# Performance work log

Hardware: AMD Instinct MI355X
Metric: run time of the kernel (lower is better)

## Reference

```python
import jax, jax.numpy as jnp
import numpy as np
from jax import lax

LATENT = 64
NUM_EMB = 512
BETA = 0.25
DN = ('NCHW', 'OIHW', 'NCHW')


def conv(x, w, b, stride, pad):
    y = lax.conv_general_dilated(x, w, (stride, stride), [(pad, pad), (pad, pad)],
                                 dimension_numbers=DN)
    return y + b[None, :, None, None]


def tconv(x, w, b, stride, pad, opad):
    # torch ConvTranspose2d(k=3, stride, padding=pad, output_padding=opad)
    # == dilated conv with lhs_dilation=stride, padding (k-1-pad, k-1-pad+opad),
    #    spatially-flipped kernel. w is stored OIHW (out, in, kh, kw).
    k = w.shape[2]
    lo, hi = k - 1 - pad, k - 1 - pad + opad
    y = lax.conv_general_dilated(x, w[:, :, ::-1, ::-1], (1, 1), [(lo, hi), (lo, hi)],
                                 lhs_dilation=(stride, stride), dimension_numbers=DN)
    return y + b[None, :, None, None]


def vector_quantize(z, codebook):
    # z: (B, D, H, W); codebook: (K, D)
    B, D, H, W = z.shape
    flat = z.transpose(0, 2, 3, 1).reshape(-1, D)  # (BHW, D)
    d = (jnp.sum(flat ** 2, axis=1, keepdims=True)
         + jnp.sum(codebook ** 2, axis=1)
         - 2.0 * flat @ codebook.T)  # (BHW, K)
    idx = jnp.argmin(d, axis=1)
    q = codebook[idx].reshape(B, H, W, D).transpose(0, 3, 1, 2)  # (B, D, H, W)
    commitment = jnp.mean((lax.stop_gradient(q) - z) ** 2)
    codebook_loss = jnp.mean((q - lax.stop_gradient(z)) ** 2)
    loss = BETA * commitment + codebook_loss
    q_ste = z + lax.stop_gradient(q - z)  # straight-through estimator
    return q_ste, loss


def setup_inputs() -> dict:
    key = jax.random.key(0)
    ks = jax.random.split(key, 16)
    f32 = jnp.float32
    inp = {
        'x': jax.random.uniform(ks[0], (1024, 1, 50, 50), dtype=f32),
        'enc_w1': jax.random.normal(ks[1], (32, 1, 3, 3), f32) * 0.1,
        'enc_b1': jnp.zeros((32,), f32),
        'enc_w2': jax.random.normal(ks[2], (64, 32, 3, 3), f32) * 0.05,
        'enc_b2': jnp.zeros((64,), f32),
        'enc_w3': jax.random.normal(ks[3], (LATENT, 64, 1, 1), f32) * 0.1,
        'enc_b3': jnp.zeros((LATENT,), f32),
        'codebook': jax.random.uniform(ks[4], (NUM_EMB, LATENT), dtype=f32),
        'dec_w1': jax.random.normal(ks[5], (64, LATENT, 3, 3), f32) * 0.05,
        'dec_b1': jnp.zeros((64,), f32),
        'dec_w2': jax.random.normal(ks[6], (32, 64, 3, 3), f32) * 0.05,
        'dec_b2': jnp.zeros((32,), f32),
        'dec_w3': jax.random.normal(ks[7], (1, 32, 3, 3), f32) * 0.05,
        'dec_b3': jnp.zeros((1,), f32),
    }
    return inp


def reference(x, enc_w1, enc_b1, enc_w2, enc_b2, enc_w3, enc_b3, codebook,
              dec_w1, dec_b1, dec_w2, dec_b2, dec_w3, dec_b3):
    # encoder: (B,1,50,50) -> (B,LATENT,13,13)
    h = jax.nn.relu(conv(x, enc_w1, enc_b1, 2, 1))
    h = jax.nn.relu(conv(h, enc_w2, enc_b2, 2, 1))
    z = conv(h, enc_w3, enc_b3, 1, 0)
    q, vq_loss = vector_quantize(z, codebook)
    # decoder: 13 -> 25 -> 50
    h = jax.nn.relu(tconv(q, dec_w1, dec_b1, 2, 1, 0))
    h = jax.nn.relu(tconv(h, dec_w2, dec_b2, 2, 1, 1))
    x_recon = jax.nn.sigmoid(conv(h, dec_w3, dec_b3, 1, 1))
    return x_recon, vq_loss
```

## Files before the change

### kernel.cpp

```cpp
#include <hip/hip_runtime.h>
#include <math.h>


typedef __attribute__((ext_vector_type(8))) short s8v;
typedef __attribute__((ext_vector_type(4))) float f4v;
typedef __attribute__((ext_vector_type(4))) int i4v;
typedef __attribute__((ext_vector_type(4))) short s4v;

__device__ inline unsigned short f2bf(float f) {
    unsigned u = __builtin_bit_cast(unsigned, f);
    return (unsigned short)((u + 0x7fffu + ((u >> 16) & 1u)) >> 16);
}
__device__ inline float bf2f(unsigned short h) {
    return __builtin_bit_cast(float, ((unsigned)h) << 16);
}

__global__ __launch_bounds__(256) void k_prep_all(
        const float* __restrict__ cb,  const float* __restrict__ ew2,
        const float* __restrict__ ew3, const float* __restrict__ dw1,
        const float* __restrict__ dw2,
        unsigned short* __restrict__ cbm, unsigned short* __restrict__ wB2n,
        unsigned short* __restrict__ wB1, unsigned short* __restrict__ wB2,
        unsigned short* __restrict__ wB3, float* __restrict__ cn,
        float* __restrict__ loss) {
    int i = blockIdx.x * 256 + threadIdx.x;
    if (i < 98304) {
        int j = i & 7, lane = (i >> 3) & 63;
        int kc = (i >> 9) % 6, nt = (i >> 9) / 6;
        int n = nt * 16 + (lane & 15);
        int k = kc * 32 + ((lane >> 4) << 3) + j;
        int seg = k >> 6, kk = k & 63;
        float c = cb[n * 64 + kk];
        unsigned short ch = f2bf(c);
        cbm[i] = (seg == 1) ? f2bf(c - bf2f(ch)) : ch;
    } else if (i < 153600) {
        int q = i - 98304;
        int j = q & 7, lane = (q >> 3) & 63;
        int kc = (q >> 9) % 27, nt = (q >> 9) / 27;
        int k = kc * 32 + ((lane >> 4) << 3) + j;
        int co = nt * 16 + (lane & 15);
        int part = (k < 288) ? 0 : (k < 576) ? 1 : 0;
        int kk = (k < 288) ? k : (k < 576) ? k - 288 : k - 576;
        int tap = kk >> 5, ci = kk & 31;
        float v = ew2[(co * 32 + ci) * 9 + tap];
        unsigned short hi = f2bf(v);
        wB2n[q] = part ? f2bf(v - bf2f(hi)) : hi;
    } else if (i < 219136) {
        int q = i - 153600;
        int j = q & 7, l = (q >> 3) & 63, kc = (q >> 9) & 7, nt = q >> 12;
        int n = nt * 16 + (l & 15), k = kc * 32 + (l >> 4) * 8 + j;
        int cls = n >> 6, co = n & 63, p = k >> 6, ci = k & 63;
        int jh = -1, jw = -1;
        if (cls == 0)      { if (p == 0) { jh = 1; jw = 1; } }
        else if (cls == 1) { if (p == 1) { jh = 1; jw = 0; } else if (p == 0) { jh = 1; jw = 2; } }
        else if (cls == 2) { if (p == 2) { jh = 0; jw = 1; } else if (p == 0) { jh = 2; jw = 1; } }
        else { if (p == 3) { jh = 0; jw = 0; } else if (p == 2) { jh = 0; jw = 2; }
               else if (p == 1) { jh = 2; jw = 0; } else { jh = 2; jw = 2; } }
        float v = (jh >= 0) ? dw1[((co * 64 + ci) * 3 + jh) * 3 + jw] : 0.f;
        wB1[q] = f2bf(v);
    } else if (i < 251904) {
        int q = i - 219136;
        int j = q & 7, l = (q >> 3) & 63, kc = (q >> 9) & 7, nt = q >> 12;
        int n = nt * 16 + (l & 15), k = kc * 32 + (l >> 4) * 8 + j;
        int cls = n >> 5, co = n & 31, p = k >> 6, ci = k & 63;
        int jh = -1, jw = -1;
        if (cls == 0)      { if (p == 0) { jh = 1; jw = 1; } }
        else if (cls == 1) { if (p == 1) { jh = 1; jw = 0; } else if (p == 0) { jh = 1; jw = 2; } }
        else if (cls == 2) { if (p == 2) { jh = 0; jw = 1; } else if (p == 0) { jh = 2; jw = 1; } }
        else { if (p == 3) { jh = 0; jw = 0; } else if (p == 2) { jh = 0; jw = 2; }
               else if (p == 1) { jh = 2; jw = 0; } else { jh = 2; jw = 2; } }
        float v = (jh >= 0) ? dw2[((co * 64 + ci) * 3 + jh) * 3 + jw] : 0.f;
        wB2[q] = f2bf(v);
    } else if (i < 264192) {
        int q = i - 251904;
        int j = q & 7, lane = (q >> 3) & 63;
        int kc = (q >> 9) % 6, nt = (q >> 9) / 6;
        int k = kc * 32 + ((lane >> 4) << 3) + j;
        int n = nt * 16 + (lane & 15);
        int part = (k < 64) ? 0 : (k < 128) ? 1 : 0;
        int kk = (k < 64) ? k : (k < 128) ? k - 64 : k - 128;
        float v = ew3[n * 64 + kk];
        unsigned short hi = f2bf(v);
        wB3[q] = part ? f2bf(v - bf2f(hi)) : hi;
    } else if (i < 264704) {
        int k = i - 264192;
        const float* r = cb + k * 64;
        float s = 0.f;
#pragma unroll
        for (int c = 0; c < 64; ++c) s += r[c] * r[c];
        cn[k] = s;
    } else if (i == 264704) {
        *loss = 0.f;
    }
}

__global__ __launch_bounds__(256) void k_conv1(const float* __restrict__ x,
                                               const float* __restrict__ w,
                                               const float* __restrict__ b,
                                               unsigned short* __restrict__ h1,
                                               int total) {
    __shared__ float4 wl4[72];
    float* wl = (float*)wl4;
    int tid = threadIdx.x;
    for (int t = tid; t < 288; t += 256) {
        int tap = t >> 5, co = t & 31;
        wl[t] = w[co * 9 + tap];
    }
    __syncthreads();
    int pix = blockIdx.x * 256 + tid;
    if (pix >= total) return;
    int n = pix / 625, p = pix % 625, oh = p / 25, ow = p % 25;
    const float* xp = x + (size_t)n * 2500;
    float4 a[8];
#pragma unroll
    for (int j = 0; j < 8; ++j) a[j] = ((const float4*)b)[j];
#pragma unroll
    for (int kh = 0; kh < 3; ++kh) {
        int ih = 2 * oh - 1 + kh;
        if ((unsigned)ih >= 50u) continue;
#pragma unroll
        for (int kw = 0; kw < 3; ++kw) {
            int iw = 2 * ow - 1 + kw;
            if ((unsigned)iw >= 50u) continue;
            float v = xp[ih * 50 + iw];
            int tap = kh * 3 + kw;
#pragma unroll
            for (int j = 0; j < 8; ++j) {
                float4 ww = wl4[tap * 8 + j];
                a[j].x += v * ww.x; a[j].y += v * ww.y;
                a[j].z += v * ww.z; a[j].w += v * ww.w;
            }
        }
    }
    unsigned short hi[32], lo[32];
#pragma unroll
    for (int j = 0; j < 8; ++j) {
        float vv[4] = {a[j].x, a[j].y, a[j].z, a[j].w};
#pragma unroll
        for (int e = 0; e < 4; ++e) {
            float v = fmaxf(vv[e], 0.f);
            unsigned short h = f2bf(v);
            hi[j * 4 + e] = h;
            lo[j * 4 + e] = f2bf(v - bf2f(h));
        }
    }
    i4v* op = (i4v*)(h1 + (size_t)pix * 64);
#pragma unroll
    for (int g = 0; g < 4; ++g) {
        i4v ph, pl;
#pragma unroll
        for (int e = 0; e < 4; ++e) {
            int b0 = g * 8 + e * 2;
            ph[e] = (int)((unsigned)hi[b0] | ((unsigned)hi[b0 + 1] << 16));
            pl[e] = (int)((unsigned)lo[b0] | ((unsigned)lo[b0 + 1] << 16));
        }
        op[g] = ph;
        op[4 + g] = pl;
    }
}

__global__ __launch_bounds__(256) void k_enc_m(const unsigned short* __restrict__ h1,
                                               const unsigned short* __restrict__ B2n,
                                               const unsigned short* __restrict__ B3,
                                               const float* __restrict__ b2,
                                               const float* __restrict__ b3,
                                               unsigned short* __restrict__ z, int npix) {
    __shared__ short a1[16 * 872];
    __shared__ short a2[16 * 200];
    __shared__ short czs[16 * 136];
    int tid = threadIdx.x, blk = blockIdx.x;
    {
        int m = tid >> 4, chunk = tid & 15;
        if (chunk < 9) {
            int pix = blk * 16 + m;
            i4v vh[4], vl[4];
#pragma unroll
            for (int g = 0; g < 4; ++g) {
                vh[g] = (i4v){0, 0, 0, 0};
                vl[g] = (i4v){0, 0, 0, 0};
            }
            if (pix < npix) {
                int n = pix / 169, p = pix % 169, oh = p / 13, ow = p % 13;
                int kh = chunk / 3, kw = chunk % 3;
                int ih = 2 * oh - 1 + kh, iw = 2 * ow - 1 + kw;
                if (((unsigned)ih < 25u) && ((unsigned)iw < 25u)) {
                    const i4v* ip = (const i4v*)(h1 + (((size_t)n * 25 + ih) * 25 + iw) * 64);
#pragma unroll
                    for (int g = 0; g < 4; ++g) { vh[g] = ip[g]; vl[g] = ip[4 + g]; }
                }
            }
            short* row = a1 + m * 872 + chunk * 32;
            i4v* d0 = (i4v*)row;
            i4v* d1 = (i4v*)(row + 288);
            i4v* d2 = (i4v*)(row + 576);
#pragma unroll
            for (int g = 0; g < 4; ++g) { d0[g] = vh[g]; d1[g] = vh[g]; d2[g] = vl[g]; }
        }
    }
    __syncthreads();
    int wave = tid >> 6, lane = tid & 63;
    int arow1 = (lane & 15) * 872 + (lane >> 4) * 8;
    f4v acc = (f4v){0.f, 0.f, 0.f, 0.f};
#pragma unroll
    for (int kc = 0; kc < 27; ++kc) {
        s8v a = *(const s8v*)(a1 + arow1 + kc * 32);
        s8v b = *(const s8v*)((const short*)B2n + ((size_t)((wave * 27 + kc) * 64 + lane)) * 8);
        acc = __builtin_amdgcn_mfma_f32_16x16x32_bf16(a, b, acc, 0, 0, 0);
    }
    {
        float bv = b2[wave * 16 + (lane & 15)];
        int n = wave * 16 + (lane & 15);
#pragma unroll
        for (int r = 0; r < 4; ++r) {
            int m = (lane >> 4) * 4 + r;
            float h = fmaxf(acc[r] + bv, 0.f);
            unsigned short hh = f2bf(h);
            unsigned short ll = f2bf(h - bf2f(hh));
            a2[m * 200 + n] = (short)hh;
            a2[m * 200 + 64 + n] = (short)hh;
            a2[m * 200 + 128 + n] = (short)ll;
        }
    }
    __syncthreads();
    int arow2 = (lane & 15) * 200 + (lane >> 4) * 8;
    f4v acc2 = (f4v){0.f, 0.f, 0.f, 0.f};
#pragma unroll
    for (int kc = 0; kc < 6; ++kc) {
        s8v a = *(const s8v*)(a2 + arow2 + kc * 32);
        s8v b = *(const s8v*)((const short*)B3 + ((size_t)((wave * 6 + kc) * 64 + lane)) * 8);
        acc2 = __builtin_amdgcn_mfma_f32_16x16x32_bf16(a, b, acc2, 0, 0, 0);
    }
    {
        float bv = b3[wave * 16 + (lane & 15)];
        int n = wave * 16 + (lane & 15);
#pragma unroll
        for (int r = 0; r < 4; ++r) {
            int m = (lane >> 4) * 4 + r;
            float v = acc2[r] + bv;
            unsigned short hh = f2bf(v);
            czs[m * 136 + n] = (short)hh;
            czs[m * 136 + 64 + n] = (short)f2bf(v - bf2f(hh));
        }
    }
    __syncthreads();
    {
        int m = tid >> 4, t = tid & 15;
        int pix = blk * 16 + m;
        if (pix < npix)
            *(i4v*)(z + (size_t)pix * 128 + t * 8) = *(i4v*)(czs + m * 136 + t * 8);
    }
}

__global__ __launch_bounds__(256, 2) void k_vq_m(const unsigned short* __restrict__ z,
                                                 const float* __restrict__ cb,
                                                 const unsigned short* __restrict__ cbm,
                                                 const float* __restrict__ cn,
                                                 unsigned short* __restrict__ q,
                                                 float* __restrict__ lpart, int npix) {
    __shared__ short a_lds[128 * 136];
    __shared__ int bkf[128];
    __shared__ float lred4[4];
    int tid = threadIdx.x, blk = blockIdx.x;
    {
        const i4v* src = (const i4v*)(z + (size_t)blk * 128 * 128);
#pragma unroll
        for (int it = 0; it < 8; ++it) {
            int L = it * 256 + tid;
            int m = L >> 4, s = L & 15;
            int pix = blk * 128 + m;
            i4v v = (i4v){0, 0, 0, 0};
            if (pix < npix) v = src[L];
            *(i4v*)(a_lds + m * 136 + s * 8) = v;
        }
    }
    __syncthreads();
    int wave = tid >> 6, lane = tid & 63;
    int arow0 = (wave * 32 + (lane & 15)) * 136 + (lane >> 4) * 8;
    int arow1 = arow0 + 16 * 136;
    s8v af00 = *(const s8v*)(a_lds + arow0);
    s8v af01 = *(const s8v*)(a_lds + arow0 + 32);
    s8v af02 = *(const s8v*)(a_lds + arow0 + 64);
    s8v af03 = *(const s8v*)(a_lds + arow0 + 96);
    s8v af10 = *(const s8v*)(a_lds + arow1);
    s8v af11 = *(const s8v*)(a_lds + arow1 + 32);
    s8v af12 = *(const s8v*)(a_lds + arow1 + 64);
    s8v af13 = *(const s8v*)(a_lds + arow1 + 96);
    float bd0[4], bd1[4];
    int bk0[4], bk1[4];
#pragma unroll
    for (int r = 0; r < 4; ++r) {
        bd0[r] = 3.4e38f; bk0[r] = 0;
        bd1[r] = 3.4e38f; bk1[r] = 0;
    }
    const s8v* bp = (const s8v*)cbm + lane;
    int ln15 = lane & 15;
    s8v bfA[6], bfB[6];
#pragma unroll
    for (int kc = 0; kc < 6; ++kc) bfA[kc] = bp[kc * 64];
    float cnA = cn[ln15];
    float cnB;
    for (int nt = 0; nt < 32; nt += 2) {
#pragma unroll
        for (int kc = 0; kc < 6; ++kc) bfB[kc] = bp[((nt + 1) * 6 + kc) * 64];
        cnB = cn[(nt + 1) * 16 + ln15];
        {
            f4v acc0 = (f4v){0.f, 0.f, 0.f, 0.f};
            f4v acc1 = (f4v){0.f, 0.f, 0.f, 0.f};
            acc0 = __builtin_amdgcn_mfma_f32_16x16x32_bf16(af00, bfA[0], acc0, 0, 0, 0);
            acc1 = __builtin_amdgcn_mfma_f32_16x16x32_bf16(af10, bfA[0], acc1, 0, 0, 0);
            acc0 = __builtin_amdgcn_mfma_f32_16x16x32_bf16(af01, bfA[1], acc0, 0, 0, 0);
            acc1 = __builtin_amdgcn_mfma_f32_16x16x32_bf16(af11, bfA[1], acc1, 0, 0, 0);
            acc0 = __builtin_amdgcn_mfma_f32_16x16x32_bf16(af00, bfA[2], acc0, 0, 0, 0);
            acc1 = __builtin_amdgcn_mfma_f32_16x16x32_bf16(af10, bfA[2], acc1, 0, 0, 0);
            acc0 = __builtin_amdgcn_mfma_f32_16x16x32_bf16(af01, bfA[3], acc0, 0, 0, 0);
            acc1 = __builtin_amdgcn_mfma_f32_16x16x32_bf16(af11, bfA[3], acc1, 0, 0, 0);
            acc0 = __builtin_amdgcn_mfma_f32_16x16x32_bf16(af02, bfA[4], acc0, 0, 0, 0);
            acc1 = __builtin_amdgcn_mfma_f32_16x16x32_bf16(af12, bfA[4], acc1, 0, 0, 0);
            acc0 = __builtin_amdgcn_mfma_f32_16x16x32_bf16(af03, bfA[5], acc0, 0, 0, 0);
            acc1 = __builtin_amdgcn_mfma_f32_16x16x32_bf16(af13, bfA[5], acc1, 0, 0, 0);
            int kcol = nt * 16 + ln15;
#pragma unroll
            for (int r = 0; r < 4; ++r) {
                float d0 = cnA - 2.f * acc0[r];
                if (d0 < bd0[r]) { bd0[r] = d0; bk0[r] = kcol; }
                float d1 = cnA - 2.f * acc1[r];
                if (d1 < bd1[r]) { bd1[r] = d1; bk1[r] = kcol; }
            }
        }
        if (nt + 2 < 32) {
#pragma unroll
            for (int kc = 0; kc < 6; ++kc) bfA[kc] = bp[((nt + 2) * 6 + kc) * 64];
            cnA = cn[(nt + 2) * 16 + ln15];
        }
        {
            f4v acc0 = (f4v){0.f, 0.f, 0.f, 0.f};
            f4v acc1 = (f4v){0.f, 0.f, 0.f, 0.f};
            acc0 = __builtin_amdgcn_mfma_f32_16x16x32_bf16(af00, bfB[0], acc0, 0, 0, 0);
            acc1 = __builtin_amdgcn_mfma_f32_16x16x32_bf16(af10, bfB[0], acc1, 0, 0, 0);
            acc0 = __builtin_amdgcn_mfma_f32_16x16x32_bf16(af01, bfB[1], acc0, 0, 0, 0);
            acc1 = __builtin_amdgcn_mfma_f32_16x16x32_bf16(af11, bfB[1], acc1, 0, 0, 0);
            acc0 = __builtin_amdgcn_mfma_f32_16x16x32_bf16(af00, bfB[2], acc0, 0, 0, 0);
            acc1 = __builtin_amdgcn_mfma_f32_16x16x32_bf16(af10, bfB[2], acc1, 0, 0, 0);
            acc0 = __builtin_amdgcn_mfma_f32_16x16x32_bf16(af01, bfB[3], acc0, 0, 0, 0);
            acc1 = __builtin_amdgcn_mfma_f32_16x16x32_bf16(af11, bfB[3], acc1, 0, 0, 0);
            acc0 = __builtin_amdgcn_mfma_f32_16x16x32_bf16(af02, bfB[4], acc0, 0, 0, 0);
            acc1 = __builtin_amdgcn_mfma_f32_16x16x32_bf16(af12, bfB[4], acc1, 0, 0, 0);
            acc0 = __builtin_amdgcn_mfma_f32_16x16x32_bf16(af03, bfB[5], acc0, 0, 0, 0);
            acc1 = __builtin_amdgcn_mfma_f32_16x16x32_bf16(af13, bfB[5], acc1, 0, 0, 0);
            int kcol = (nt + 1) * 16 + ln15;
#pragma unroll
            for (int r = 0; r < 4; ++r) {
                float d0 = cnB - 2.f * acc0[r];
                if (d0 < bd0[r]) { bd0[r] = d0; bk0[r] = kcol; }
                float d1 = cnB - 2.f * acc1[r];
                if (d1 < bd1[r]) { bd1[r] = d1; bk1[r] = kcol; }
            }
        }
    }
#pragma unroll
    for (int off = 1; off < 16; off <<= 1) {
#pragma unroll
        for (int r = 0; r < 4; ++r) {
            float od = __shfl_xor(bd0[r], off);
            int ok = __shfl_xor(bk0[r], off);
            if (od < bd0[r] || (od == bd0[r] && ok < bk0[r])) { bd0[r] = od; bk0[r] = ok; }
            od = __shfl_xor(bd1[r], off);
            ok = __shfl_xor(bk1[r], off);
            if (od < bd1[r] || (od == bd1[r] && ok < bk1[r])) { bd1[r] = od; bk1[r] = ok; }
        }
    }
    if ((lane & 15) == 0) {
#pragma unroll
        for (int r = 0; r < 4; ++r) {
            bkf[wave * 32 + (lane >> 4) * 4 + r] = bk0[r];
            bkf[wave * 32 + 16 + (lane >> 4) * 4 + r] = bk1[r];
        }
    }
    __syncthreads();
    float lsum = 0.f;
#pragma unroll
    for (int it = 0; it < 8; ++it) {
        int L = it * 256 + tid;
        int m = L >> 4, c4 = L & 15;
        int pix = blk * 128 + m;
        if (pix < npix) {
            int k0 = bkf[m];
            float4 cq = ((const float4*)cb)[(size_t)k0 * 16 + c4];
            const short* rz = a_lds + m * 136 + c4 * 4;
            s4v zh4 = *(const s4v*)rz;
            s4v zl4 = *(const s4v*)(rz + 64);
            float zx = bf2f((unsigned short)zh4[0]) + bf2f((unsigned short)zl4[0]);
            float zy = bf2f((unsigned short)zh4[1]) + bf2f((unsigned short)zl4[1]);
            float zz = bf2f((unsigned short)zh4[2]) + bf2f((unsigned short)zl4[2]);
            float zw = bf2f((unsigned short)zh4[3]) + bf2f((unsigned short)zl4[3]);
            float dx = cq.x - zx, dy = cq.y - zy, dz = cq.z - zz, dw = cq.w - zw;
            lsum += dx * dx + dy * dy + dz * dz + dw * dw;
            s4v qs;
            qs[0] = (short)f2bf(cq.x); qs[1] = (short)f2bf(cq.y);
            qs[2] = (short)f2bf(cq.z); qs[3] = (short)f2bf(cq.w);
            *(s4v*)(q + (size_t)pix * 64 + c4 * 4) = qs;
        }
    }
#pragma unroll
    for (int off = 32; off > 0; off >>= 1) lsum += __shfl_down(lsum, off);
    if (lane == 0) lred4[wave] = lsum;
    __syncthreads();
    if (tid == 0) lpart[blk] = lred4[0] + lred4[1] + lred4[2] + lred4[3];
}

__global__ __launch_bounds__(256) void k_loss(const float* __restrict__ lpart,
                                              int nblk, float* __restrict__ loss) {
    int tid = threadIdx.x;
    float s = 0.f;
    for (int i = tid; i < nblk; i += 256) s += lpart[i];
#pragma unroll
    for (int off = 32; off > 0; off >>= 1) s += __shfl_down(s, off);
    __shared__ float w4[4];
    if ((tid & 63) == 0) w4[tid >> 6] = s;
    __syncthreads();
    if (tid == 0)
        atomicAdd(loss, (w4[0] + w4[1] + w4[2] + w4[3]) * (1.25f / 11075584.f));
}

__global__ __launch_bounds__(256) void k_tconv1_m(const unsigned short* __restrict__ q,
                                                  const unsigned short* __restrict__ wB,
                                                  const float* __restrict__ bias,
                                                  unsigned short* __restrict__ d1,
                                                  int nquad) {
    __shared__ short a_lds[32 * 264];
    __shared__ short c_lds[32 * 264];
    int tid = threadIdx.x, blk = blockIdx.x;
#pragma unroll
    for (int pass = 0; pass < 4; ++pass) {
        int idx = tid + pass * 256;
        int m = idx >> 5, sub = idx & 31;
        int qg = blk * 32 + m;
        int p = sub >> 3, ci0 = (sub & 7) * 8;
        i4v v = (i4v){0, 0, 0, 0};
        if (qg < nquad) {
            int img = qg / 169, r = qg % 169, qm = r / 13, qw = r % 13;
            int sm = qm + (p >> 1), sw = qw + (p & 1);
            if (sm < 13 && sw < 13)
                v = *(const i4v*)(q + (((size_t)img * 13 + sm) * 13 + sw) * 64 + ci0);
        }
        *(i4v*)(a_lds + m * 264 + sub * 8) = v;
    }
    __syncthreads();
    int wave = tid >> 6, lane = tid & 63;
    f4v acc[2][4];
#pragma unroll
    for (int mt = 0; mt < 2; ++mt)
#pragma unroll
        for (int i = 0; i < 4; ++i) acc[mt][i] = (f4v){0.f, 0.f, 0.f, 0.f};
    float bv[4];
#pragma unroll
    for (int i = 0; i < 4; ++i) bv[i] = bias[((wave * 4 + i) * 16 + (lane & 15)) & 63];
#pragma unroll
    for (int kc = 0; kc < 8; ++kc) {
        s8v a0 = *(const s8v*)(a_lds + ((lane & 15)) * 264 + (lane >> 4) * 8 + kc * 32);
        s8v a1 = *(const s8v*)(a_lds + (16 + (lane & 15)) * 264 + (lane >> 4) * 8 + kc * 32);
#pragma unroll
        for (int i = 0; i < 4; ++i) {
            int nt = wave * 4 + i;
            s8v b = *(const s8v*)((const short*)wB + ((size_t)((nt * 8 + kc) * 64 + lane)) * 8);
            acc[0][i] = __builtin_amdgcn_mfma_f32_16x16x32_bf16(a0, b, acc[0][i], 0, 0, 0);
            acc[1][i] = __builtin_amdgcn_mfma_f32_16x16x32_bf16(a1, b, acc[1][i], 0, 0, 0);
        }
    }
#pragma unroll
    for (int mt = 0; mt < 2; ++mt)
#pragma unroll
        for (int i = 0; i < 4; ++i) {
            int n = (wave * 4 + i) * 16 + (lane & 15);
#pragma unroll
            for (int r2 = 0; r2 < 4; ++r2) {
                int m = mt * 16 + (lane >> 4) * 4 + r2;
                float v = fmaxf(acc[mt][i][r2] + bv[i], 0.f);
                c_lds[m * 264 + n] = (short)f2bf(v);
            }
        }
    __syncthreads();
#pragma unroll
    for (int pass = 0; pass < 4; ++pass) {
        int ch = tid + pass * 256;
        int m = ch >> 5, cpart = ch & 31;
        int qg = blk * 32 + m;
        if (qg >= nquad) continue;
        int img = qg / 169, r = qg % 169, qm = r / 13, qw = r % 13;
        int cls = cpart >> 3, co8 = (cpart & 7) * 8;
        int oh = 2 * qm + (cls >> 1), ow = 2 * qw + (cls & 1);
        if (oh >= 25 || ow >= 25) continue;
        i4v val = *(i4v*)(c_lds + m * 264 + cls * 64 + co8);
        *(i4v*)(d1 + (((size_t)img * 25 + oh) * 25 + ow) * 64 + co8) = val;
    }
}

__global__ __launch_bounds__(256) void k_tconv2_m(const unsigned short* __restrict__ d1,
                                                  const unsigned short* __restrict__ wB,
                                                  const float* __restrict__ bias,
                                                  unsigned short* __restrict__ d2,
                                                  int nquad) {
    __shared__ short a_lds[32 * 264];
    __shared__ short c_lds[32 * 136];
    int tid = threadIdx.x, blk = blockIdx.x;
#pragma unroll
    for (int pass = 0; pass < 4; ++pass) {
        int idx = tid + pass * 256;
        int m = idx >> 5, sub = idx & 31;
        int qg = blk * 32 + m;
        int p = sub >> 3, ci0 = (sub & 7) * 8;
        i4v v = (i4v){0, 0, 0, 0};
        if (qg < nquad) {
            int img = qg / 625, r = qg % 625, qm = r / 25, qw = r % 25;
            int sm = qm + (p >> 1), sw = qw + (p & 1);
            if (sm < 25 && sw < 25)
                v = *(const i4v*)(d1 + (((size_t)img * 25 + sm) * 25 + sw) * 64 + ci0);
        }
        *(i4v*)(a_lds + m * 264 + sub * 8) = v;
    }
    __syncthreads();
    int wave = tid >> 6, lane = tid & 63;
    f4v acc[2][2];
#pragma unroll
    for (int mt = 0; mt < 2; ++mt)
#pragma unroll
        for (int i = 0; i < 2; ++i) acc[mt][i] = (f4v){0.f, 0.f, 0.f, 0.f};
    float bv[2];
#pragma unroll
    for (int i = 0; i < 2; ++i) bv[i] = bias[((wave * 2 + i) * 16 + (lane & 15)) & 31];
#pragma unroll
    for (int kc = 0; kc < 8; ++kc) {
        s8v a0 = *(const s8v*)(a_lds + ((lane & 15)) * 264 + (lane >> 4) * 8 + kc * 32);
        s8v a1 = *(const s8v*)(a_lds + (16 + (lane & 15)) * 264 + (lane >> 4) * 8 + kc * 32);
#pragma unroll
        for (int i = 0; i < 2; ++i) {
            int nt = wave * 2 + i;
            s8v b = *(const s8v*)((const short*)wB + ((size_t)((nt * 8 + kc) * 64 + lane)) * 8);
            acc[0][i] = __builtin_amdgcn_mfma_f32_16x16x32_bf16(a0, b, acc[0][i], 0, 0, 0);
            acc[1][i] = __builtin_amdgcn_mfma_f32_16x16x32_bf16(a1, b, acc[1][i], 0, 0, 0);
        }
    }
#pragma unroll
    for (int mt = 0; mt < 2; ++mt)
#pragma unroll
        for (int i = 0; i < 2; ++i) {
            int n = (wave * 2 + i) * 16 + (lane & 15);
#pragma unroll
            for (int r2 = 0; r2 < 4; ++r2) {
                int m = mt * 16 + (lane >> 4) * 4 + r2;
                float v = fmaxf(acc[mt][i][r2] + bv[i], 0.f);
                c_lds[m * 136 + n] = (short)f2bf(v);
            }
        }
    __syncthreads();
#pragma unroll
    for (int pass = 0; pass < 2; ++pass) {
        int ch = tid + pass * 256;
        int m = ch >> 4, cpart = ch & 15;
        int qg = blk * 32 + m;
        if (qg >= nquad) continue;
        int img = qg / 625, r = qg % 625, qm = r / 25, qw = r % 25;
        int cls = cpart >> 2, co8 = (cpart & 3) * 8;
        int oh = 2 * qm + (cls >> 1), ow = 2 * qw + (cls & 1);
        i4v val = *(i4v*)(c_lds + m * 136 + cls * 32 + co8);
        *(i4v*)(d2 + (((size_t)img * 50 + oh) * 50 + ow) * 32 + co8) = val;
    }
}

__global__ __launch_bounds__(256) void k_convf(const unsigned short* __restrict__ in,
                                               const float* __restrict__ w,
                                               const float* __restrict__ b,
                                               float* __restrict__ out, int total) {
    __shared__ float wl[288];
    int tid = threadIdx.x;
    for (int t = tid; t < 288; t += 256) {
        int tap = t >> 5, ci = t & 31;
        wl[t] = w[ci * 9 + tap];
    }
    __syncthreads();
    int pix = blockIdx.x * 256 + tid;
    if (pix >= total) return;
    int n = pix / 2500, p = pix % 2500, oh = p / 50, ow = p % 50;
    float acc = b[0];
#pragma unroll
    for (int kh = 0; kh < 3; ++kh) {
        int ih = oh - 1 + kh;
        if ((unsigned)ih >= 50u) continue;
#pragma unroll
        for (int kw = 0; kw < 3; ++kw) {
            int iw = ow - 1 + kw;
            if ((unsigned)iw >= 50u) continue;
            const float* wt = wl + (kh * 3 + kw) * 32;
            const i4v* ip4 = (const i4v*)(in + (((size_t)n * 50 + ih) * 50 + iw) * 32);
#pragma unroll
            for (int c8 = 0; c8 < 4; ++c8) {
                i4v u = ip4[c8];
#pragma unroll
                for (int e = 0; e < 4; ++e) {
                    unsigned uu = (unsigned)u[e];
                    float x0 = __builtin_bit_cast(float, uu << 16);
                    float x1 = __builtin_bit_cast(float, uu & 0xffff0000u);
                    acc = fmaf(x0, wt[c8 * 8 + e * 2], acc);
                    acc = fmaf(x1, wt[c8 * 8 + e * 2 + 1], acc);
                }
            }
        }
    }
    out[pix] = 1.f / (1.f + expf(-acc));
}

extern "C" void kernel_launch(void* const* d_in, const int* in_sizes, int n_in,
                              void* d_out, int out_size, void* d_ws, size_t ws_size,
                              hipStream_t stream) {
    const float* x   = (const float*)d_in[0];
    const float* ew1 = (const float*)d_in[1];
    const float* eb1 = (const float*)d_in[2];
    const float* ew2 = (const float*)d_in[3];
    const float* eb2 = (const float*)d_in[4];
    const float* ew3 = (const float*)d_in[5];
    const float* eb3 = (const float*)d_in[6];
    const float* cb  = (const float*)d_in[7];
    const float* dw1 = (const float*)d_in[8];
    const float* db1 = (const float*)d_in[9];
    const float* dw2 = (const float*)d_in[10];
    const float* db2 = (const float*)d_in[11];
    const float* dw3 = (const float*)d_in[12];
    const float* db3 = (const float*)d_in[13];
    float* out = (float*)d_out;
    float* loss = out + 2560000;

    float* ws = (float*)d_ws;
    float* cn = ws;
    unsigned short* wB1  = (unsigned short*)(ws + 512);
    unsigned short* wB2  = (unsigned short*)(ws + 33280);
    unsigned short* wB2n = (unsigned short*)(ws + 49664);
    unsigned short* wB3  = (unsigned short*)(ws + 77312);
    unsigned short* cbm  = (unsigned short*)(ws + 83456);
    float* lpart = ws + 132608;
    const size_t tw_floats = 133968;

    const int B = 1024;
    const size_t A_per = 40000, B_per = 20000;
    size_t avail = (ws_size / 4 > tw_floats) ? ws_size / 4 - tw_floats : 0;
    int BC = (int)(avail / (A_per + B_per));
    if (BC > B) BC = B;
    if (BC < 1) BC = 1;
    float* regA = ws + tw_floats;
    float* regB = regA + (size_t)BC * A_per;

    k_prep_all<<<1035, 256, 0, stream>>>(cb, ew2, ew3, dw1, dw2,
                                         cbm, wB2n, wB1, wB2, wB3, cn, loss);

    for (int n0 = 0; n0 < B; n0 += BC) {
        int bc = (B - n0 < BC) ? (B - n0) : BC;
        const float* xch = x + (size_t)n0 * 2500;

        int t1 = bc * 625;
        unsigned short* h1p = (unsigned short*)regA;
        k_conv1<<<(t1 + 255) / 256, 256, 0, stream>>>(xch, ew1, eb1, h1p, t1);

        int npix = bc * 169;
        unsigned short* zp = (unsigned short*)regB;
        k_enc_m<<<(npix + 15) / 16, 256, 0, stream>>>(h1p, wB2n, wB3, eb2, eb3, zp, npix);

        unsigned short* qb = (unsigned short*)regA;
        int nblk = (npix + 127) / 128;
        k_vq_m<<<nblk, 256, 0, stream>>>(zp, cb, cbm, cn, qb, lpart, npix);

        k_loss<<<1, 256, 0, stream>>>(lpart, nblk, loss);

        unsigned short* d1 = (unsigned short*)regB;
        k_tconv1_m<<<(npix + 31) / 32, 256, 0, stream>>>(qb, wB1, db1, d1, npix);

        int nq2 = bc * 625;
        unsigned short* d2 = (unsigned short*)regA;
        k_tconv2_m<<<(nq2 + 31) / 32, 256, 0, stream>>>(d1, wB2, db2, d2, nq2);

        int t6 = bc * 2500;
        k_convf<<<(t6 + 255) / 256, 256, 0, stream>>>(d2, dw3, db3, out + (size_t)n0 * 2500, t6);
    }
}
```

Before: 459.4 us.

## Register-block final 3x3 conv over 10-row strips with packed weights

Rewrites the final 32->1 conv so each thread computes a strip of 10 output rows in one column. Each loaded input row is reused across all three kernel rows, cutting redundant global loads. Weights are prepacked as float2 pairs in the prep kernel and held in registers, and accumulation uses packed float2 math. The cost is tenfold fewer threads and higher register pressure, which may reduce latency hiding.

Result: no change. 452.1 us (-1.6%).

```diff
diff --git a/kernel.cpp b/kernel.cpp
--- a/kernel.cpp
+++ b/kernel.cpp
@@ -6,6 +6,7 @@
 typedef __attribute__((ext_vector_type(4))) float f4v;
 typedef __attribute__((ext_vector_type(4))) int i4v;
 typedef __attribute__((ext_vector_type(4))) short s4v;
+typedef __attribute__((ext_vector_type(2))) float f2v;
 
 __device__ inline unsigned short f2bf(float f) {
     unsigned u = __builtin_bit_cast(unsigned, f);
@@ -18,11 +19,11 @@
 __global__ __launch_bounds__(256) void k_prep_all(
         const float* __restrict__ cb,  const float* __restrict__ ew2,
         const float* __restrict__ ew3, const float* __restrict__ dw1,
-        const float* __restrict__ dw2,
+        const float* __restrict__ dw2, const float* __restrict__ dw3,
         unsigned short* __restrict__ cbm, unsigned short* __restrict__ wB2n,
         unsigned short* __restrict__ wB1, unsigned short* __restrict__ wB2,
         unsigned short* __restrict__ wB3, float* __restrict__ cn,
-        float* __restrict__ loss) {
+        float* __restrict__ loss, f2v* __restrict__ wpk) {
     int i = blockIdx.x * 256 + threadIdx.x;
     if (i < 98304) {
         int j = i & 7, lane = (i >> 3) & 63;
@@ -91,6 +92,13 @@
         cn[k] = s;
     } else if (i == 264704) {
         *loss = 0.f;
+    } else if (i < 264849) {
+        int q = i - 264705;
+        int kw = q / 48, rem = q % 48, kh = rem / 16, ii = rem % 16;
+        f2v w;
+        w[0] = dw3[(2 * ii) * 9 + kh * 3 + kw];
+        w[1] = dw3[(2 * ii + 1) * 9 + kh * 3 + kw];
+        wpk[q] = w;
     }
 }
 
@@ -567,46 +575,58 @@
     }
 }
 
-__global__ __launch_bounds__(256) void k_convf(const unsigned short* __restrict__ in,
-                                               const float* __restrict__ w,
-                                               const float* __restrict__ b,
-                                               float* __restrict__ out, int total) {
-    __shared__ float wl[288];
-    int tid = threadIdx.x;
-    for (int t = tid; t < 288; t += 256) {
-        int tap = t >> 5, ci = t & 31;
-        wl[t] = w[ci * 9 + tap];
-    }
-    __syncthreads();
-    int pix = blockIdx.x * 256 + tid;
-    if (pix >= total) return;
-    int n = pix / 2500, p = pix % 2500, oh = p / 50, ow = p % 50;
-    float acc = b[0];
-#pragma unroll
-    for (int kh = 0; kh < 3; ++kh) {
-        int ih = oh - 1 + kh;
-        if ((unsigned)ih >= 50u) continue;
-#pragma unroll
-        for (int kw = 0; kw < 3; ++kw) {
-            int iw = ow - 1 + kw;
-            if ((unsigned)iw >= 50u) continue;
-            const float* wt = wl + (kh * 3 + kw) * 32;
-            const i4v* ip4 = (const i4v*)(in + (((size_t)n * 50 + ih) * 50 + iw) * 32);
+__global__ __launch_bounds__(256, 2) void k_convf(const unsigned short* __restrict__ in,
+                                                  const f2v* __restrict__ wpk,
+                                                  const float* __restrict__ b,
+                                                  float* __restrict__ out, int nthr) {
+    int t = blockIdx.x * 256 + threadIdx.x;
+    if (t >= nthr) return;
+    int img = t / 250, r = t % 250;
+    int strip = r / 50, col = r % 50;
+    int r0 = strip * 10;
+    const unsigned short* base = in + (size_t)img * 80000;
+    f2v acc[10];
+#pragma unroll
+    for (int i = 0; i < 10; ++i) acc[i] = (f2v){0.f, 0.f};
+    for (int dx = -1; dx <= 1; ++dx) {
+        int ic = col + dx;
+        if ((unsigned)ic >= 50u) continue;
+        int kw = dx + 1;
+        const f2v* wp = wpk + kw * 48;
+        f2v w2r[3][16];
+#pragma unroll
+        for (int kh = 0; kh < 3; ++kh)
+#pragma unroll
+            for (int i = 0; i < 16; ++i) w2r[kh][i] = wp[kh * 16 + i];
+#pragma unroll
+        for (int rr = -1; rr <= 10; ++rr) {
+            int ih = r0 + rr;
+            if ((unsigned)ih >= 50u) continue;
+            const i4v* px = (const i4v*)(base + ((size_t)ih * 50 + ic) * 32);
 #pragma unroll
             for (int c8 = 0; c8 < 4; ++c8) {
-                i4v u = ip4[c8];
+                i4v u = px[c8];
 #pragma unroll
                 for (int e = 0; e < 4; ++e) {
                     unsigned uu = (unsigned)u[e];
-                    float x0 = __builtin_bit_cast(float, uu << 16);
-                    float x1 = __builtin_bit_cast(float, uu & 0xffff0000u);
-                    acc = fmaf(x0, wt[c8 * 8 + e * 2], acc);
-                    acc = fmaf(x1, wt[c8 * 8 + e * 2 + 1], acc);
+                    f2v x;
+                    x[0] = __builtin_bit_cast(float, uu << 16);
+                    x[1] = __builtin_bit_cast(float, uu & 0xffff0000u);
+                    int i = c8 * 4 + e;
+                    if (rr - 1 >= 0 && rr - 1 <= 9) acc[rr - 1] += x * w2r[2][i];
+                    if (rr >= 0 && rr <= 9)         acc[rr]     += x * w2r[1][i];
+                    if (rr + 1 >= 0 && rr + 1 <= 9) acc[rr + 1] += x * w2r[0][i];
                 }
             }
         }
     }
-    out[pix] = 1.f / (1.f + expf(-acc));
+    float b0 = b[0];
+    float* op = out + (size_t)img * 2500 + (size_t)r0 * 50 + col;
+#pragma unroll
+    for (int i = 0; i < 10; ++i) {
+        float v = acc[i][0] + acc[i][1] + b0;
+        op[(size_t)i * 50] = 1.f / (1.f + expf(-v));
+    }
 }
 
 extern "C" void kernel_launch(void* const* d_in, const int* in_sizes, int n_in,
@@ -637,7 +657,8 @@
     unsigned short* wB3  = (unsigned short*)(ws + 77312);
     unsigned short* cbm  = (unsigned short*)(ws + 83456);
     float* lpart = ws + 132608;
-    const size_t tw_floats = 133968;
+    f2v* wpk = (f2v*)(ws + 133968);
+    const size_t tw_floats = 134256;
 
     const int B = 1024;
     const size_t A_per = 40000, B_per = 20000;
@@ -648,8 +669,8 @@
     float* regA = ws + tw_floats;
     float* regB = regA + (size_t)BC * A_per;
 
-    k_prep_all<<<1035, 256, 0, stream>>>(cb, ew2, ew3, dw1, dw2,
-                                         cbm, wB2n, wB1, wB2, wB3, cn, loss);
+    k_prep_all<<<1035, 256, 0, stream>>>(cb, ew2, ew3, dw1, dw2, dw3,
+                                         cbm, wB2n, wB1, wB2, wB3, cn, loss, wpk);
 
     for (int n0 = 0; n0 < B; n0 += BC) {
         int bc = (B - n0 < BC) ? (B - n0) : BC;
@@ -676,7 +697,7 @@
         unsigned short* d2 = (unsigned short*)regA;
         k_tconv2_m<<<(nq2 + 31) / 32, 256, 0, stream>>>(d1, wB2, db2, d2, nq2);
 
-        int t6 = bc * 2500;
-        k_convf<<<(t6 + 255) / 256, 256, 0, stream>>>(d2, dw3, db3, out + (size_t)n0 * 2500, t6);
-    }
-}
+        int t6 = bc * 250;
+        k_convf<<<(t6 + 255) / 256, 256, 0, stream>>>(d2, wpk, db3, out + (size_t)n0 * 2500, t6);
+    }
+}
```
